# Kernel tuning notes

Measured on AMD Instinct MI355X. Metric: run time of the kernel, lower is better.

Reference implementation:

```python
import jax, jax.numpy as jnp
import numpy as np

T_DIM, BATCH, D_DATA, H_HID = 128, 512, 512, 512
EPS = 1e-8  # torch cosine_similarity eps


def setup_inputs() -> dict:
    key = jax.random.key(0)
    k1, k2, k3, k4, k5 = jax.random.split(key, 5)
    s = 1.0 / np.sqrt(H_HID)  # torch LSTM default init scale
    return {
        "X_tilde": jax.random.normal(k1, (BATCH, T_DIM, D_DATA), jnp.float32),
        "W_ih": jax.random.normal(k2, (4 * H_HID, D_DATA), jnp.float32) * s,
        "W_hh": jax.random.normal(k3, (4 * H_HID, H_HID), jnp.float32) * s,
        "b_ih": jax.random.normal(k4, (4 * H_HID,), jnp.float32) * s,
        "b_hh": jax.random.normal(k5, (4 * H_HID,), jnp.float32) * s,
    }


def _ta_forward(X_tilde, W_ih, W_hh, b_ih, b_hh):
    B, T, D = X_tilde.shape
    H = W_hh.shape[1]

    def lstm_step(carry, x_t):  # x_t: [B, D]
        h, c = carry
        gates = x_t @ W_ih.T + h @ W_hh.T + (b_ih + b_hh)  # [B, 4H]
        i, f, g, o = jnp.split(gates, 4, axis=-1)  # torch gate order i,f,g,o
        i, f, o = jax.nn.sigmoid(i), jax.nn.sigmoid(f), jax.nn.sigmoid(o)
        g = jnp.tanh(g)
        c = f * c + i * g
        h = o * jnp.tanh(c)
        return (h, c), h

    h0 = jnp.zeros((B, H), X_tilde.dtype)
    c0 = jnp.zeros((B, H), X_tilde.dtype)
    # only the first T-1 inputs are fed to the LSTM (last hidden stored pre-step)
    xs = jnp.swapaxes(X_tilde[:, : T - 1, :], 0, 1)  # [T-1, B, D]
    _, hs = jax.lax.scan(lstm_step, (h0, c0), xs)  # [T-1, B, H]
    hidden_tensor = jnp.concatenate([h0[None], hs], axis=0)  # [T, B, H]

    # cosine similarity of each prior hidden (flattened over batch*H) vs final hidden
    ht_prior = hidden_tensor[:-1].reshape(T - 1, -1)  # [T-1, B*H]
    ht_fin = hidden_tensor[-1].reshape(-1)  # [B*H]
    num = ht_prior @ ht_fin  # [T-1]
    denom = jnp.maximum(jnp.linalg.norm(ht_prior, axis=1), EPS) * \
            jnp.maximum(jnp.linalg.norm(ht_fin), EPS)
    alpha = jax.nn.softmax(num / denom, axis=0)  # [T-1]

    ht_final = jnp.sum(alpha[:, None, None] * hidden_tensor[:-1], axis=0)  # [B, H]
    return ht_final[None]  # [1, B, H]


def reference(X_tilde, W_ih, W_hh, b_ih, b_hh):
    return _ta_forward(X_tilde, W_ih, W_hh, b_ih, b_hh)
```

## Files before the change

kernel.cpp:

```cpp
#include <hip/hip_runtime.h>
#include <stdint.h>

#define T_DIM  128
#define TSTEPS 127
#define BATCH  512
#define DDATA  512
#define HHID   512
#define BH     262144
#define CPAD   132

typedef _Float16 f16;
typedef _Float16 f16x8 __attribute__((ext_vector_type(8)));
typedef float    f32x4 __attribute__((ext_vector_type(4)));
typedef unsigned int u32x2 __attribute__((ext_vector_type(2)));

#define MFMA16 __builtin_amdgcn_mfma_f32_16x16x32_f16

__device__ __forceinline__ f16x8 ld16(const f16* p) {
  f16x8 r;
  asm volatile("global_load_dwordx4 %0, %1, off" : "=v"(r) : "v"(p));
  return r;
}
__device__ __forceinline__ f16x8 ld16cc(const f16* p) {
  f16x8 r;
  asm volatile("global_load_dwordx4 %0, %1, off sc0 sc1" : "=v"(r) : "v"(p));
  return r;
}
__device__ __forceinline__ void st8cc(void* p, u32x2 v) {
  asm volatile("global_store_dwordx2 %0, %1, off sc0 sc1" :: "v"(p), "v"(v) : "memory");
}

__global__ void k_prep_w(const float* __restrict__ W_ih, const float* __restrict__ W_hh,
                         f16* __restrict__ W16B) {
  int d = blockIdx.x * blockDim.x + threadIdx.x;
  int lane = d & 63;
  int fi   = (d >> 6) & 31;
  int ch   = (d >> 11) & 1;
  int kq   = (d >> 12) & 3;
  int nbv  = d >> 14;
  int ks = fi >> 2, nf = fi & 3;
  int col16 = lane & 15, lk2 = lane >> 4;
  int hm = col16 >> 2, g = col16 & 3;
  int hg = nbv * 32 + (ch * 4 + nf) * 4 + hm;
  int R = g * 512 + hg;
  int k = kq * 256 + ks * 32 + lk2 * 8;
  const float* src = (k < 512) ? (W_ih + (size_t)R * 512 + k)
                               : (W_hh + (size_t)R * 512 + (k - 512));
  f16x8 o;
#pragma unroll
  for (int e = 0; e < 8; e++) o[e] = (f16)src[e];
  *(f16x8*)(W16B + (size_t)d * 8) = o;
}

__global__ void k_prep_b(const float* __restrict__ b_ih, const float* __restrict__ b_hh,
                         float* __restrict__ biasR) {
  int r = blockIdx.x * blockDim.x + threadIdx.x;
  if (r < 2048) biasR[r] = b_ih[r] + b_hh[r];
}

__global__ void k_prep_x(const float* __restrict__ X, f16* __restrict__ XT) {
  int c = blockIdx.x * blockDim.x + threadIdx.x;
  int t   = c >> 15;
  int rem = c & 32767;
  int kc  = rem >> 9;
  int row = rem & 511;
  const float* src = X + (size_t)row * (T_DIM * DDATA) + t * DDATA + kc * 8;
  f16x8 o;
#pragma unroll
  for (int e = 0; e < 8; e++) o[e] = (f16)src[e];
  *(f16x8*)(XT + (size_t)t * BH + kc * 4096 + row * 8) = o;
}

__launch_bounds__(512, 1)
__global__ void k_lstm(const f16* __restrict__ XT, f16* __restrict__ h_all,
                       const f16* __restrict__ W16B, const float* __restrict__ biasR,
                       int* __restrict__ done) {
  __shared__ float C[4][32][CPAD];
  __shared__ float BiasS[128];
  __shared__ int goS;

  const int tid = threadIdx.x, lane = tid & 63, w = tid >> 6;
  const int kq = w >> 1;
  const int wg = blockIdx.x;
  const int mb = (wg & 7) * 2 + ((wg >> 3) & 1);
  const int nb = wg >> 4;
  const int m0 = mb * 32;
  const int l15 = lane & 15, lk = lane >> 4;

  f16x8 B[32];
  {
    const f16* wb = W16B + ((size_t)((nb * 4 + kq) * 2 + (w & 1)) * 32) * 512 + lane * 8;
#pragma unroll
    for (int i = 0; i < 32; i++) B[i] = ld16(wb + i * 512);
    asm volatile("s_waitcnt vmcnt(0)" ::: "memory");
    __builtin_amdgcn_sched_barrier(0);
  }
  if (tid < 128) {
    int q8 = tid >> 4, hm = (tid >> 2) & 3, g = tid & 3;
    BiasS[tid] = biasR[g * 512 + nb * 32 + q8 * 4 + hm];
  }
  if (tid == 0) goS = 0;
  float c_reg[4] = {0.f, 0.f, 0.f, 0.f};
  __syncthreads();

#define WAITV(N) asm volatile("s_waitcnt vmcnt(" #N ")" ::: "memory");        \
                 __builtin_amdgcn_sched_barrier(0)
#define MFMA4KS(KS0)                                                          \
    {                                                                         \
      _Pragma("unroll")                                                       \
      for (int s = 0; s < 4; s++) {                                           \
        int ks = KS0 + s;                                                     \
        _Pragma("unroll")                                                     \
        for (int nf = 0; nf < 4; nf++) {                                      \
          acc[0][nf] = MFMA16(R[2 * ks],     B[ks * 4 + nf], acc[0][nf], 0, 0, 0); \
          acc[1][nf] = MFMA16(R[2 * ks + 1], B[ks * 4 + nf], acc[1][nf], 0, 0, 0); \
        }                                                                     \
      }                                                                       \
    }
#define ISSUE_X(T)                                                            \
    {                                                                         \
      const f16* Ab = XT + (size_t)(T) * BH + (size_t)(kq * 32 + lk) * 4096   \
                      + (size_t)(m0 + l15) * 8;                               \
      _Pragma("unroll")                                                       \
      for (int ks = 0; ks < 8; ks++) {                                        \
        R[2 * ks]     = ld16(Ab + (size_t)ks * 16384);                        \
        R[2 * ks + 1] = ld16(Ab + (size_t)ks * 16384 + 128);                  \
      }                                                                       \
    }

  f16x8 R[16];
  if (kq < 2) ISSUE_X(0);

  for (int t = 0; t < TSTEPS; t++) {
    f32x4 acc[2][4] = {};

    if (kq < 2) {
      WAITV(0);
      MFMA4KS(0);
      MFMA4KS(4);
      if (t + 1 < TSTEPS) ISSUE_X(t + 1);
    } else if (t > 0) {
      if (w == 4) {
        if (lane == 0) {
          const int* flag = done + (size_t)(mb * 128 + (t - 1)) * 16;
          int spins = 0;
          while (__hip_atomic_load(flag, __ATOMIC_RELAXED, __HIP_MEMORY_SCOPE_AGENT) < 16) {
            __builtin_amdgcn_s_sleep(1);
            if (++spins > (1 << 22)) break;
          }
          __hip_atomic_store(&goS, t, __ATOMIC_RELAXED, __HIP_MEMORY_SCOPE_WORKGROUP);
        }
      } else {
        int spins = 0;
        while (__hip_atomic_load(&goS, __ATOMIC_RELAXED, __HIP_MEMORY_SCOPE_WORKGROUP) < t) {
          __builtin_amdgcn_s_sleep(1);
          if (++spins > (1 << 22)) break;
        }
      }
      const f16* Hb = h_all + (size_t)t * BH + (size_t)((kq - 2) * 32 + lk) * 4096
                      + (size_t)(m0 + l15) * 8;
#pragma unroll
      for (int ks = 0; ks < 8; ks++) {
        R[2 * ks]     = ld16cc(Hb + (size_t)ks * 16384);
        R[2 * ks + 1] = ld16cc(Hb + (size_t)ks * 16384 + 128);
      }
      WAITV(8);  MFMA4KS(0);
      WAITV(0);  MFMA4KS(4);
    }

#pragma unroll
    for (int mf = 0; mf < 2; mf++)
#pragma unroll
      for (int nf = 0; nf < 4; nf++)
#pragma unroll
        for (int r = 0; r < 4; r++)
          C[kq][mf * 16 + lk * 4 + r][(w & 1) * 64 + nf * 16 + l15] = acc[mf][nf][r];
    __syncthreads();

    if (tid < 256) {
      int r = tid >> 3, q8 = tid & 7;
      f32x4 uu[4] = {};
#pragma unroll
      for (int q = 0; q < 4; q++) {
        const f32x4* base = (const f32x4*)&C[q][r][q8 * 16];
        uu[0] += base[0];
        uu[1] += base[1];
        uu[2] += base[2];
        uu[3] += base[3];
      }
      union { f16 h[4]; u32x2 v; } pk;
#pragma unroll
      for (int hm = 0; hm < 4; hm++) {
        float gi = uu[hm][0] + BiasS[q8 * 16 + hm * 4 + 0];
        float gf = uu[hm][1] + BiasS[q8 * 16 + hm * 4 + 1];
        float gg = uu[hm][2] + BiasS[q8 * 16 + hm * 4 + 2];
        float go = uu[hm][3] + BiasS[q8 * 16 + hm * 4 + 3];
        float ii = 1.f / (1.f + __expf(-gi));
        float ff = 1.f / (1.f + __expf(-gf));
        float eg = __expf(-2.f * fabsf(gg));
        float tg = copysignf((1.f - eg) / (1.f + eg), gg);
        float oo = 1.f / (1.f + __expf(-go));
        c_reg[hm] = ff * c_reg[hm] + ii * tg;
        float ec = __expf(-2.f * fabsf(c_reg[hm]));
        float th = copysignf((1.f - ec) / (1.f + ec), c_reg[hm]);
        pk.h[hm] = (f16)(oo * th);
      }
      f16* dst = h_all + (size_t)(t + 1) * BH
                 + (size_t)(nb * 4 + (q8 >> 1)) * 4096 + (size_t)(m0 + r) * 8
                 + (q8 & 1) * 4;
      st8cc(dst, pk.v);
    }
    asm volatile("s_waitcnt vmcnt(0)" ::: "memory");
    __syncthreads();
    if (tid == 0)
      __hip_atomic_fetch_add(done + (size_t)(mb * 128 + t) * 16, 1,
                             __ATOMIC_RELAXED, __HIP_MEMORY_SCOPE_AGENT);
  }
#undef WAITV
#undef MFMA4KS
#undef ISSUE_X
}

__global__ void k_dots(const f16* __restrict__ h_all, float* __restrict__ part) {
  int t = blockIdx.x, s = blockIdx.y;
  const f16x8* ht = (const f16x8*)(h_all + (size_t)t * BH) + (size_t)s * 8192;
  const f16x8* hf = (const f16x8*)(h_all + (size_t)127 * BH) + (size_t)s * 8192;
  float sn = 0.f, sq = 0.f;
  for (int i = threadIdx.x; i < 8192; i += 256) {
    f16x8 a = ht[i], b = hf[i];
#pragma unroll
    for (int e = 0; e < 8; e++) {
      float fa = (float)a[e], fb = (float)b[e];
      sn += fa * fb; sq += fa * fa;
    }
  }
  for (int off = 32; off; off >>= 1) {
    sn += __shfl_down(sn, off);
    sq += __shfl_down(sq, off);
  }
  __shared__ float red[8];
  int wid = threadIdx.x >> 6;
  if ((threadIdx.x & 63) == 0) { red[wid] = sn; red[4 + wid] = sq; }
  __syncthreads();
  if (threadIdx.x == 0) {
    part[t * 8 + s]     = red[0] + red[1] + red[2] + red[3];
    part[t * 8 + 4 + s] = red[4] + red[5] + red[6] + red[7];
  }
}

__global__ void k_softmax(float* __restrict__ part) {
  __shared__ float sn_s[128], sq_s[128];
  int t = threadIdx.x;
  if (t < 128) {
    float sn = part[t * 8 + 0] + part[t * 8 + 1] + part[t * 8 + 2] + part[t * 8 + 3];
    float sq = part[t * 8 + 4] + part[t * 8 + 5] + part[t * 8 + 6] + part[t * 8 + 7];
    sn_s[t] = sn; sq_s[t] = sq;
  }
  __syncthreads();
  if (t == 0) {
    float nf = fmaxf(sqrtf(sq_s[127]), 1e-8f);
    float m = -1e30f;
    for (int i = 0; i < TSTEPS; i++) {
      float np = fmaxf(sqrtf(sq_s[i]), 1e-8f);
      sn_s[i] = sn_s[i] / (np * nf);
      m = fmaxf(m, sn_s[i]);
    }
    float ssum = 0.f;
    for (int i = 0; i < TSTEPS; i++) { float e = __expf(sn_s[i] - m); sn_s[i] = e; ssum += e; }
    float inv = 1.f / ssum;
    for (int i = 0; i < TSTEPS; i++) part[1024 + i] = sn_s[i] * inv;
  }
}

__global__ void k_out(const f16* __restrict__ h_all, const float* __restrict__ part,
                      float* __restrict__ out) {
  __shared__ float al[TSTEPS];
  if (threadIdx.x < TSTEPS) al[threadIdx.x] = part[1024 + threadIdx.x];
  __syncthreads();
  int g = blockIdx.x * blockDim.x + threadIdx.x;
  int kc = g >> 9, row = g & 511;
  float s[8] = {0.f, 0.f, 0.f, 0.f, 0.f, 0.f, 0.f, 0.f};
  for (int t = 1; t < TSTEPS; t++) {
    f16x8 v = *(const f16x8*)(h_all + (size_t)t * BH + (size_t)kc * 4096 + row * 8);
    float a = al[t];
#pragma unroll
    for (int e = 0; e < 8; e++) s[e] += a * (float)v[e];
  }
  float* o = out + (size_t)row * 512 + kc * 8;
  f32x4 lo = {s[0], s[1], s[2], s[3]}, hi = {s[4], s[5], s[6], s[7]};
  *(f32x4*)o = lo;
  *(f32x4*)(o + 4) = hi;
}

extern "C" void kernel_launch(void* const* d_in, const int* in_sizes, int n_in,
                              void* d_out, int out_size, void* d_ws, size_t ws_size,
                              hipStream_t stream) {
  const float* X    = (const float*)d_in[0];
  const float* W_ih = (const float*)d_in[1];
  const float* W_hh = (const float*)d_in[2];
  const float* b_ih = (const float*)d_in[3];
  const float* b_hh = (const float*)d_in[4];

  char* ws = (char*)d_ws;
  size_t off = 0;
  auto alloc = [&](size_t bytes) -> void* {
    void* p = ws + off;
    off = (off + bytes + 255) & ~(size_t)255;
    return p;
  };
  f16*   W16B  = (f16*)  alloc((size_t)2048 * 1024 * 2);
  float* biasR = (float*)alloc(2048 * 4);
  f16*   XT    = (f16*)  alloc((size_t)TSTEPS * BH * 2);
  f16*   h_all = (f16*)  alloc((size_t)T_DIM * BH * 2);
  int*   done  = (int*)  alloc(16 * 128 * 16 * 4);
  float* part  = (float*)alloc(2048 * 4);

  hipMemsetAsync(h_all, 0, (size_t)BH * 2, stream);
  hipMemsetAsync(done,  0, 16 * 128 * 16 * 4, stream);

  k_prep_w<<<1024, 256, 0, stream>>>(W_ih, W_hh, W16B);
  k_prep_b<<<8, 256, 0, stream>>>(b_ih, b_hh, biasR);
  k_prep_x<<<(TSTEPS * 512 * 64) / 256, 256, 0, stream>>>(X, XT);

  k_lstm<<<256, 512, 0, stream>>>(XT, h_all, W16B, biasR, done);

  k_dots<<<dim3(128, 4), 256, 0, stream>>>(h_all, part);
  k_softmax<<<1, 128, 0, stream>>>(part);
  k_out<<<128, 256, 0, stream>>>(h_all, part, (float*)d_out);
}
```

Before: 617.8 us.

## Replace counter flags with sentinel-polled hidden state and tile X transpose through LDS

Drops the per-step atomic done counters and the leader-wave spin. The h_all buffer is pre-filled with a 0xFF sentinel (f16 NaN), and the recurrent waves poll the hidden-state loads directly until no sentinel words remain. This removes the store-wait, the extra barrier and the flag round trip on the critical path of each step. The X preparation kernel now stages rows in LDS for coalesced reads and writes. The change relies on 32-bit writes landing whole and on a computed h never matching the sentinel pattern, and it adds a large memset plus repeated reloads while polling.

```diff
diff --git a/kernel.cpp b/kernel.cpp
--- a/kernel.cpp
+++ b/kernel.cpp
@@ -29,6 +29,8 @@
 __device__ __forceinline__ void st8cc(void* p, u32x2 v) {
   asm volatile("global_store_dwordx2 %0, %1, off sc0 sc1" :: "v"(p), "v"(v) : "memory");
 }
+
+#define BAR_LGKM do { asm volatile("s_waitcnt lgkmcnt(0)\n\ts_barrier" ::: "memory"); } while (0)
 
 __global__ void k_prep_w(const float* __restrict__ W_ih, const float* __restrict__ W_hh,
                          f16* __restrict__ W16B) {
@@ -59,25 +61,46 @@
 }
 
 __global__ void k_prep_x(const float* __restrict__ X, f16* __restrict__ XT) {
-  int c = blockIdx.x * blockDim.x + threadIdx.x;
-  int t   = c >> 15;
-  int rem = c & 32767;
-  int kc  = rem >> 9;
-  int row = rem & 511;
-  const float* src = X + (size_t)row * (T_DIM * DDATA) + t * DDATA + kc * 8;
-  f16x8 o;
-#pragma unroll
-  for (int e = 0; e < 8; e++) o[e] = (f16)src[e];
-  *(f16x8*)(XT + (size_t)t * BH + kc * 4096 + row * 8) = o;
+  __shared__ f16 Ls[32][516];
+  const int t = blockIdx.x;
+  const int rb = blockIdx.y;
+  const int tid = threadIdx.x;
+  const int rloc = tid >> 5;
+  const int dc = (tid & 31) * 16;
+#pragma unroll
+  for (int it = 0; it < 4; it++) {
+    int row = it * 8 + rloc;
+    const float* src = X + (size_t)(rb * 32 + row) * (T_DIM * DDATA)
+                         + (size_t)t * DDATA + dc;
+    f32x4 a0 = *(const f32x4*)(src);
+    f32x4 a1 = *(const f32x4*)(src + 4);
+    f32x4 a2 = *(const f32x4*)(src + 8);
+    f32x4 a3 = *(const f32x4*)(src + 12);
+    f16x8 h0, h1;
+#pragma unroll
+    for (int e = 0; e < 4; e++) {
+      h0[e] = (f16)a0[e]; h0[4 + e] = (f16)a1[e];
+      h1[e] = (f16)a2[e]; h1[4 + e] = (f16)a3[e];
+    }
+    *(f16x8*)&Ls[row][dc] = h0;
+    *(f16x8*)&Ls[row][dc + 8] = h1;
+  }
+  __syncthreads();
+#pragma unroll
+  for (int it = 0; it < 8; it++) {
+    int chunk = it * 256 + tid;
+    int kc = chunk >> 5, row = chunk & 31;
+    f16x8 v = *(const f16x8*)&Ls[row][kc * 8];
+    *(f16x8*)(XT + (size_t)t * BH + (size_t)kc * 4096
+              + (size_t)(rb * 32 + row) * 8) = v;
+  }
 }
 
 __launch_bounds__(512, 1)
 __global__ void k_lstm(const f16* __restrict__ XT, f16* __restrict__ h_all,
-                       const f16* __restrict__ W16B, const float* __restrict__ biasR,
-                       int* __restrict__ done) {
+                       const f16* __restrict__ W16B, const float* __restrict__ biasR) {
   __shared__ float C[4][32][CPAD];
   __shared__ float BiasS[128];
-  __shared__ int goS;
 
   const int tid = threadIdx.x, lane = tid & 63, w = tid >> 6;
   const int kq = w >> 1;
@@ -99,7 +122,6 @@
     int q8 = tid >> 4, hm = (tid >> 2) & 3, g = tid & 3;
     BiasS[tid] = biasR[g * 512 + nb * 32 + q8 * 4 + hm];
   }
-  if (tid == 0) goS = 0;
   float c_reg[4] = {0.f, 0.f, 0.f, 0.f};
   __syncthreads();
 
@@ -140,32 +162,28 @@
       MFMA4KS(4);
       if (t + 1 < TSTEPS) ISSUE_X(t + 1);
     } else if (t > 0) {
-      if (w == 4) {
-        if (lane == 0) {
-          const int* flag = done + (size_t)(mb * 128 + (t - 1)) * 16;
-          int spins = 0;
-          while (__hip_atomic_load(flag, __ATOMIC_RELAXED, __HIP_MEMORY_SCOPE_AGENT) < 16) {
-            __builtin_amdgcn_s_sleep(1);
-            if (++spins > (1 << 22)) break;
-          }
-          __hip_atomic_store(&goS, t, __ATOMIC_RELAXED, __HIP_MEMORY_SCOPE_WORKGROUP);
-        }
-      } else {
-        int spins = 0;
-        while (__hip_atomic_load(&goS, __ATOMIC_RELAXED, __HIP_MEMORY_SCOPE_WORKGROUP) < t) {
-          __builtin_amdgcn_s_sleep(1);
-          if (++spins > (1 << 22)) break;
-        }
-      }
       const f16* Hb = h_all + (size_t)t * BH + (size_t)((kq - 2) * 32 + lk) * 4096
                       + (size_t)(m0 + l15) * 8;
-#pragma unroll
-      for (int ks = 0; ks < 8; ks++) {
-        R[2 * ks]     = ld16cc(Hb + (size_t)ks * 16384);
-        R[2 * ks + 1] = ld16cc(Hb + (size_t)ks * 16384 + 128);
+      int rounds = 0;
+      while (true) {
+#pragma unroll
+        for (int ks = 0; ks < 8; ks++) {
+          R[2 * ks]     = ld16cc(Hb + (size_t)ks * 16384);
+          R[2 * ks + 1] = ld16cc(Hb + (size_t)ks * 16384 + 128);
+        }
+        WAITV(0);
+        unsigned bad = 0;
+#pragma unroll
+        for (int i = 0; i < 16; i++) {
+          const unsigned* u = (const unsigned*)&R[i];
+          bad |= (unsigned)(u[0] == 0xFFFFFFFFu) | (unsigned)(u[2] == 0xFFFFFFFFu);
+        }
+        if (__all(bad == 0)) break;
+        if (++rounds > 4096) break;
+        __builtin_amdgcn_s_sleep(1);
       }
-      WAITV(8);  MFMA4KS(0);
-      WAITV(0);  MFMA4KS(4);
+      MFMA4KS(0);
+      MFMA4KS(4);
     }
 
 #pragma unroll
@@ -175,7 +193,7 @@
 #pragma unroll
         for (int r = 0; r < 4; r++)
           C[kq][mf * 16 + lk * 4 + r][(w & 1) * 64 + nf * 16 + l15] = acc[mf][nf][r];
-    __syncthreads();
+    BAR_LGKM;
 
     if (tid < 256) {
       int r = tid >> 3, q8 = tid & 7;
@@ -210,11 +228,7 @@
                  + (q8 & 1) * 4;
       st8cc(dst, pk.v);
     }
-    asm volatile("s_waitcnt vmcnt(0)" ::: "memory");
-    __syncthreads();
-    if (tid == 0)
-      __hip_atomic_fetch_add(done + (size_t)(mb * 128 + t) * 16, 1,
-                             __ATOMIC_RELAXED, __HIP_MEMORY_SCOPE_AGENT);
+    BAR_LGKM;
   }
 #undef WAITV
 #undef MFMA4KS
@@ -312,17 +326,16 @@
   float* biasR = (float*)alloc(2048 * 4);
   f16*   XT    = (f16*)  alloc((size_t)TSTEPS * BH * 2);
   f16*   h_all = (f16*)  alloc((size_t)T_DIM * BH * 2);
-  int*   done  = (int*)  alloc(16 * 128 * 16 * 4);
   float* part  = (float*)alloc(2048 * 4);
 
   hipMemsetAsync(h_all, 0, (size_t)BH * 2, stream);
-  hipMemsetAsync(done,  0, 16 * 128 * 16 * 4, stream);
+  hipMemsetAsync(h_all + BH, 0xFF, (size_t)TSTEPS * BH * 2, stream);
 
   k_prep_w<<<1024, 256, 0, stream>>>(W_ih, W_hh, W16B);
   k_prep_b<<<8, 256, 0, stream>>>(b_ih, b_hh, biasR);
-  k_prep_x<<<(TSTEPS * 512 * 64) / 256, 256, 0, stream>>>(X, XT);
-
-  k_lstm<<<256, 512, 0, stream>>>(XT, h_all, W16B, biasR, done);
+  k_prep_x<<<dim3(TSTEPS, 16), 256, 0, stream>>>(X, XT);
+
+  k_lstm<<<256, 512, 0, stream>>>(XT, h_all, W16B, biasR);
 
   k_dots<<<dim3(128, 4), 256, 0, stream>>>(h_all, part);
   k_softmax<<<1, 128, 0, stream>>>(part);
```

New measurement: 631.8 us. 1.02x slower.
